# Kernel optimization log

Measured on AMD Instinct MI355X. Metric: run time of the kernel, lower is better.

Reference implementation:

```python
import jax, jax.numpy as jnp
import numpy as np

NUM_GRAPHS = 1024
N_NODES = 8388608

def setup_inputs() -> dict:
    key = jax.random.key(0)
    k1, k2, k3 = jax.random.split(key, 3)
    positions = jax.random.normal(k1, (N_NODES, 3), dtype=jnp.float32)
    q = jax.random.normal(k2, (N_NODES,), dtype=jnp.float32)
    batch = jnp.sort(jax.random.randint(k3, (N_NODES,), 0, NUM_GRAPHS, dtype=jnp.int64))
    return {"positions": positions, "q": q, "batch": batch}

def reference(positions, q, batch):
    # q: [N] -> [N,1]; remove global mean over all nodes (remove_mean=True)
    qc = q[:, None] - jnp.mean(q)
    # per-graph polarization: sum_i q_i * r_i  -> [NUM_GRAPHS, 3]
    pol = jax.ops.segment_sum(qc * positions, batch, num_segments=NUM_GRAPHS)
    return pol
```

## Files before the change

kernel.cpp:

```cpp
#include <hip/hip_runtime.h>


#define N_NODES         8388608
#define NUM_GRAPHS      1024
#define BLK             256
#define NODES_PER_BLOCK 4096
#define NBLOCKS         (N_NODES / NODES_PER_BLOCK)
#define CHUNK_NODES     1024
#define NCHUNK          (NODES_PER_BLOCK / CHUNK_NODES)
#define CHUNK_F4        (CHUNK_NODES * 3 / 4)
#define PAD4(u)         ((u) + ((u) >> 3))
#define LDS_F4          (CHUNK_F4 + (CHUNK_F4 >> 3))
#define NSLOT           4

#define IBASE_OFF       16
#define REC_OFF         2064
#define REC_STRIDE      32
#define EXTRA_OFF       (REC_OFF + NBLOCKS * REC_STRIDE)
#define WS_FLOATS       (EXTRA_OFF + NUM_GRAPHS * 6)

__global__ __launch_bounds__(BLK) void pol_main(const float4* __restrict__ p4,
                                                const float4* __restrict__ q4,
                                                const int4*   __restrict__ b4,
                                                const int*    __restrict__ batch,
                                                float* __restrict__ ws) {
    __shared__ float4 spos[LDS_F4];
    __shared__ float  sslot[NSLOT * 6];
    __shared__ float  sqsum;

    const int t = threadIdx.x;
    const int b = blockIdx.x;
    float* extra = ws + EXTRA_OFF;

    if (t == 0) sqsum = 0.f;
    if (t < NSLOT * 6) sslot[t] = 0.f;
    const int base = batch[b * NODES_PER_BLOCK];

    int idA = -1, idB = -1;
    float aqx = 0, aqy = 0, aqz = 0, arx = 0, ary = 0, arz = 0;
    float bqx = 0, bqy = 0, bqz = 0, brx = 0, bry = 0, brz = 0;
    float qsum = 0.f;

    const int blk_f4 = b * (NODES_PER_BLOCK * 3 / 4);
    const int blk_v4 = b * (NODES_PER_BLOCK / 4);

    for (int c = 0; c < NCHUNK; ++c) {
        #pragma unroll
        for (int k = 0; k < 3; ++k) {
            int u = t + BLK * k;
            spos[PAD4(u)] = p4[blk_f4 + c * CHUNK_F4 + u];
        }
        __syncthreads();

        int vi = blk_v4 + c * (CHUNK_NODES / 4) + t;
        float4 qv = q4[vi];
        int4   bv = b4[vi];
        int u0 = 3 * t;
        float4 p0 = spos[PAD4(u0)];
        float4 p1 = spos[PAD4(u0 + 1)];
        float4 p2 = spos[PAD4(u0 + 2)];

        float qs[4] = {qv.x, qv.y, qv.z, qv.w};
        int   ids[4] = {bv.x, bv.y, bv.z, bv.w};
        float px[4] = {p0.x, p0.w, p1.z, p2.y};
        float py[4] = {p0.y, p1.x, p1.w, p2.z};
        float pz[4] = {p0.z, p1.y, p2.x, p2.w};

        #pragma unroll
        for (int j = 0; j < 4; ++j) {
            float qj = qs[j];
            int   id = ids[j];
            qsum += qj;
            if (id == idA) {
                aqx = fmaf(qj, px[j], aqx); aqy = fmaf(qj, py[j], aqy); aqz = fmaf(qj, pz[j], aqz);
                arx += px[j]; ary += py[j]; arz += pz[j];
            } else if (id == idB) {
                bqx = fmaf(qj, px[j], bqx); bqy = fmaf(qj, py[j], bqy); bqz = fmaf(qj, pz[j], bqz);
                brx += px[j]; bry += py[j]; brz += pz[j];
            } else if (idA < 0) {
                idA = id;
                aqx = qj * px[j]; aqy = qj * py[j]; aqz = qj * pz[j];
                arx = px[j]; ary = py[j]; arz = pz[j];
            } else if (idB < 0) {
                idB = id;
                bqx = qj * px[j]; bqy = qj * py[j]; bqz = qj * pz[j];
                brx = px[j]; bry = py[j]; brz = pz[j];
            } else {
                atomicAdd(&extra[idA * 6 + 0], aqx); atomicAdd(&extra[idA * 6 + 1], aqy);
                atomicAdd(&extra[idA * 6 + 2], aqz); atomicAdd(&extra[idA * 6 + 3], arx);
                atomicAdd(&extra[idA * 6 + 4], ary); atomicAdd(&extra[idA * 6 + 5], arz);
                idA = id;
                aqx = qj * px[j]; aqy = qj * py[j]; aqz = qj * pz[j];
                arx = px[j]; ary = py[j]; arz = pz[j];
            }
        }
        __syncthreads();
    }

    #pragma unroll
    for (int off = 32; off > 0; off >>= 1) qsum += __shfl_down(qsum, off, 64);
    if ((t & 63) == 0) atomicAdd(&sqsum, qsum);

    {
        int s = idA - base;
        if (s < NSLOT) {
            atomicAdd(&sslot[s * 6 + 0], aqx); atomicAdd(&sslot[s * 6 + 1], aqy);
            atomicAdd(&sslot[s * 6 + 2], aqz); atomicAdd(&sslot[s * 6 + 3], arx);
            atomicAdd(&sslot[s * 6 + 4], ary); atomicAdd(&sslot[s * 6 + 5], arz);
        } else {
            atomicAdd(&extra[idA * 6 + 0], aqx); atomicAdd(&extra[idA * 6 + 1], aqy);
            atomicAdd(&extra[idA * 6 + 2], aqz); atomicAdd(&extra[idA * 6 + 3], arx);
            atomicAdd(&extra[idA * 6 + 4], ary); atomicAdd(&extra[idA * 6 + 5], arz);
        }
    }
    if (idB >= 0) {
        int s = idB - base;
        if (s < NSLOT) {
            atomicAdd(&sslot[s * 6 + 0], bqx); atomicAdd(&sslot[s * 6 + 1], bqy);
            atomicAdd(&sslot[s * 6 + 2], bqz); atomicAdd(&sslot[s * 6 + 3], brx);
            atomicAdd(&sslot[s * 6 + 4], bry); atomicAdd(&sslot[s * 6 + 5], brz);
        } else {
            atomicAdd(&extra[idB * 6 + 0], bqx); atomicAdd(&extra[idB * 6 + 1], bqy);
            atomicAdd(&extra[idB * 6 + 2], bqz); atomicAdd(&extra[idB * 6 + 3], brx);
            atomicAdd(&extra[idB * 6 + 4], bry); atomicAdd(&extra[idB * 6 + 5], brz);
        }
    }
    __syncthreads();

    float* rec = ws + REC_OFF + (size_t)b * REC_STRIDE;
    if (t == 0) {
        rec[0] = sqsum;
        ((int*)(ws + IBASE_OFF))[b] = base;
    }
    if (t < NSLOT * 6) rec[8 + t] = sslot[t];
}

__global__ __launch_bounds__(BLK) void mean_kernel(float* __restrict__ ws) {
    __shared__ float sm[4];
    float s = 0.f;
    for (int i = threadIdx.x; i < NBLOCKS; i += BLK) s += ws[REC_OFF + (size_t)i * REC_STRIDE];
    #pragma unroll
    for (int off = 32; off > 0; off >>= 1) s += __shfl_down(s, off, 64);
    int lane = threadIdx.x & 63, wave = threadIdx.x >> 6;
    if (lane == 0) sm[wave] = s;
    __syncthreads();
    if (threadIdx.x == 0) ws[0] = ((sm[0] + sm[1]) + (sm[2] + sm[3])) * (1.0f / (float)N_NODES);
}

__global__ __launch_bounds__(BLK) void finalize_kernel(const float* __restrict__ ws,
                                                       float* __restrict__ out) {
    int g = blockIdx.x * BLK + threadIdx.x;
    if (g >= NUM_GRAPHS) return;
    const float mean = ws[0];
    const int* ibase = (const int*)(ws + IBASE_OFF);
    const float* extra = ws + EXTRA_OFF;

    float qx = extra[g * 6 + 0], qy = extra[g * 6 + 1], qz = extra[g * 6 + 2];
    float rx = extra[g * 6 + 3], ry = extra[g * 6 + 4], rz = extra[g * 6 + 5];

    int lo = 0, hi = NBLOCKS - 1, B = -1;
    while (lo <= hi) {
        int mid = (lo + hi) >> 1;
        if (ibase[mid] <= g) { B = mid; lo = mid + 1; } else hi = mid - 1;
    }
    for (int b = B; b >= 0; --b) {
        int s = g - ibase[b];
        if (s >= NSLOT) break;
        const float* sl = ws + REC_OFF + (size_t)b * REC_STRIDE + 8 + s * 6;
        qx += sl[0]; qy += sl[1]; qz += sl[2];
        rx += sl[3]; ry += sl[4]; rz += sl[5];
    }
    out[g * 3 + 0] = fmaf(-mean, rx, qx);
    out[g * 3 + 1] = fmaf(-mean, ry, qy);
    out[g * 3 + 2] = fmaf(-mean, rz, qz);
}


__global__ void sum_q_kernel(const float* __restrict__ q, float* __restrict__ ws, int n4) {
    int tid = blockIdx.x * blockDim.x + threadIdx.x;
    int stride = gridDim.x * blockDim.x;
    const float4* q4 = (const float4*)q;
    float s = 0.f;
    for (int i = tid; i < n4; i += stride) {
        float4 v = q4[i];
        s += (v.x + v.y) + (v.z + v.w);
    }
    for (int off = 32; off > 0; off >>= 1) s += __shfl_down(s, off, 64);
    __shared__ float smem[4];
    int lane = threadIdx.x & 63, wave = threadIdx.x >> 6;
    if (lane == 0) smem[wave] = s;
    __syncthreads();
    if (threadIdx.x == 0) atomicAdd(ws, (smem[0] + smem[1]) + (smem[2] + smem[3]));
}

__global__ void pol_atomic_kernel(const float* __restrict__ pos,
                                  const float* __restrict__ q,
                                  const int*   __restrict__ batch,
                                  const float* __restrict__ ws,
                                  float* __restrict__ out, int n) {
    const float mean = ws[0] * (1.0f / (float)N_NODES);
    int tid = blockIdx.x * blockDim.x + threadIdx.x;
    int stride = gridDim.x * blockDim.x;
    int n4 = n >> 2;
    const float4* q4 = (const float4*)q;
    const int4*   b4 = (const int4*)batch;
    const float4* p4 = (const float4*)pos;

    for (int i = tid; i < n4; i += stride) {
        float4 qv = q4[i];
        int4   bv = b4[i];
        float4 p0 = p4[3 * i + 0];
        float4 p1 = p4[3 * i + 1];
        float4 p2 = p4[3 * i + 2];
        float qs[4] = {qv.x - mean, qv.y - mean, qv.z - mean, qv.w - mean};
        int  ids[4] = {bv.x, bv.y, bv.z, bv.w};
        float px[4] = {p0.x, p0.w, p1.z, p2.y};
        float py[4] = {p0.y, p1.x, p1.w, p2.z};
        float pz[4] = {p0.z, p1.y, p2.x, p2.w};
        int cur = ids[0];
        float sx = 0.f, sy = 0.f, sz = 0.f;
        #pragma unroll
        for (int j = 0; j < 4; ++j) {
            if (ids[j] != cur) {
                atomicAdd(&out[cur * 3 + 0], sx);
                atomicAdd(&out[cur * 3 + 1], sy);
                atomicAdd(&out[cur * 3 + 2], sz);
                sx = sy = sz = 0.f;
                cur = ids[j];
            }
            sx = fmaf(qs[j], px[j], sx);
            sy = fmaf(qs[j], py[j], sy);
            sz = fmaf(qs[j], pz[j], sz);
        }
        int first = __shfl(cur, 0, 64);
        bool uniform = __all(cur == first);
        if (uniform) {
            for (int off = 32; off > 0; off >>= 1) {
                sx += __shfl_down(sx, off, 64);
                sy += __shfl_down(sy, off, 64);
                sz += __shfl_down(sz, off, 64);
            }
            if ((threadIdx.x & 63) == 0) {
                atomicAdd(&out[cur * 3 + 0], sx);
                atomicAdd(&out[cur * 3 + 1], sy);
                atomicAdd(&out[cur * 3 + 2], sz);
            }
        } else {
            atomicAdd(&out[cur * 3 + 0], sx);
            atomicAdd(&out[cur * 3 + 1], sy);
            atomicAdd(&out[cur * 3 + 2], sz);
        }
    }
}

extern "C" void kernel_launch(void* const* d_in, const int* in_sizes, int n_in,
                              void* d_out, int out_size, void* d_ws, size_t ws_size,
                              hipStream_t stream) {
    const float* pos   = (const float*)d_in[0];
    const float* q     = (const float*)d_in[1];
    const int*   batch = (const int*)d_in[2];
    float* out = (float*)d_out;
    float* ws  = (float*)d_ws;
    int n = in_sizes[1];

    if (ws_size >= (size_t)WS_FLOATS * sizeof(float)) {
        hipMemsetAsync(ws + EXTRA_OFF, 0, (size_t)NUM_GRAPHS * 6 * sizeof(float), stream);
        pol_main<<<NBLOCKS, BLK, 0, stream>>>((const float4*)pos, (const float4*)q,
                                              (const int4*)batch, batch, ws);
        mean_kernel<<<1, BLK, 0, stream>>>(ws);
        finalize_kernel<<<NUM_GRAPHS / BLK, BLK, 0, stream>>>(ws, out);
    } else {
        hipMemsetAsync(d_out, 0, (size_t)out_size * sizeof(float), stream);
        hipMemsetAsync(d_ws, 0, sizeof(float), stream);
        sum_q_kernel<<<4096, BLK, 0, stream>>>(q, ws, n >> 2);
        pol_atomic_kernel<<<8192, BLK, 0, stream>>>(pos, q, batch, ws, out, n);
    }
}
```

Baseline: 222.8 us.

## Load positions directly, wave-reduce uniform segments, fuse mean into finalize

Removes the LDS staging of positions and its per-chunk barriers, so each thread reads its three float4 position words straight from global memory, which are contiguous per thread rather than coalesced across the wave. Before flushing, segment accumulators are reduced across the wave with shuffles when all lanes hold the same graph id, which cuts the number of shared and global atomics. The mean kernel is merged into a single 1024-thread finalize kernel, removing one launch. The risks are less efficient strided global access patterns and the extra ballot and shuffle work.

```diff
diff --git a/kernel.cpp b/kernel.cpp
--- a/kernel.cpp
+++ b/kernel.cpp
@@ -6,11 +6,7 @@
 #define BLK             256
 #define NODES_PER_BLOCK 4096
 #define NBLOCKS         (N_NODES / NODES_PER_BLOCK)
-#define CHUNK_NODES     1024
-#define NCHUNK          (NODES_PER_BLOCK / CHUNK_NODES)
-#define CHUNK_F4        (CHUNK_NODES * 3 / 4)
-#define PAD4(u)         ((u) + ((u) >> 3))
-#define LDS_F4          (CHUNK_F4 + (CHUNK_F4 >> 3))
+#define ITER            4
 #define NSLOT           4
 
 #define IBASE_OFF       16
@@ -19,14 +15,29 @@
 #define EXTRA_OFF       (REC_OFF + NBLOCKS * REC_STRIDE)
 #define WS_FLOATS       (EXTRA_OFF + NUM_GRAPHS * 6)
 
+__device__ __forceinline__ void flush_seg(int id, int base,
+                                          float qx, float qy, float qz,
+                                          float rx, float ry, float rz,
+                                          float* sslot, float* extra) {
+    int s = id - base;
+    if (s < NSLOT) {
+        atomicAdd(&sslot[s * 6 + 0], qx); atomicAdd(&sslot[s * 6 + 1], qy);
+        atomicAdd(&sslot[s * 6 + 2], qz); atomicAdd(&sslot[s * 6 + 3], rx);
+        atomicAdd(&sslot[s * 6 + 4], ry); atomicAdd(&sslot[s * 6 + 5], rz);
+    } else {
+        atomicAdd(&extra[id * 6 + 0], qx); atomicAdd(&extra[id * 6 + 1], qy);
+        atomicAdd(&extra[id * 6 + 2], qz); atomicAdd(&extra[id * 6 + 3], rx);
+        atomicAdd(&extra[id * 6 + 4], ry); atomicAdd(&extra[id * 6 + 5], rz);
+    }
+}
+
 __global__ __launch_bounds__(BLK) void pol_main(const float4* __restrict__ p4,
                                                 const float4* __restrict__ q4,
                                                 const int4*   __restrict__ b4,
                                                 const int*    __restrict__ batch,
                                                 float* __restrict__ ws) {
-    __shared__ float4 spos[LDS_F4];
-    __shared__ float  sslot[NSLOT * 6];
-    __shared__ float  sqsum;
+    __shared__ float sslot[NSLOT * 6];
+    __shared__ float sqsum;
 
     const int t = threadIdx.x;
     const int b = blockIdx.x;
@@ -35,30 +46,23 @@
     if (t == 0) sqsum = 0.f;
     if (t < NSLOT * 6) sslot[t] = 0.f;
     const int base = batch[b * NODES_PER_BLOCK];
+    __syncthreads();
 
     int idA = -1, idB = -1;
     float aqx = 0, aqy = 0, aqz = 0, arx = 0, ary = 0, arz = 0;
     float bqx = 0, bqy = 0, bqz = 0, brx = 0, bry = 0, brz = 0;
     float qsum = 0.f;
 
-    const int blk_f4 = b * (NODES_PER_BLOCK * 3 / 4);
     const int blk_v4 = b * (NODES_PER_BLOCK / 4);
 
-    for (int c = 0; c < NCHUNK; ++c) {
-        #pragma unroll
-        for (int k = 0; k < 3; ++k) {
-            int u = t + BLK * k;
-            spos[PAD4(u)] = p4[blk_f4 + c * CHUNK_F4 + u];
-        }
-        __syncthreads();
-
-        int vi = blk_v4 + c * (CHUNK_NODES / 4) + t;
+    #pragma unroll
+    for (int j = 0; j < ITER; ++j) {
+        int vi = blk_v4 + j * BLK + t;
         float4 qv = q4[vi];
         int4   bv = b4[vi];
-        int u0 = 3 * t;
-        float4 p0 = spos[PAD4(u0)];
-        float4 p1 = spos[PAD4(u0 + 1)];
-        float4 p2 = spos[PAD4(u0 + 2)];
+        float4 p0 = p4[3 * vi + 0];
+        float4 p1 = p4[3 * vi + 1];
+        float4 p2 = p4[3 * vi + 2];
 
         float qs[4] = {qv.x, qv.y, qv.z, qv.w};
         int   ids[4] = {bv.x, bv.y, bv.z, bv.w};
@@ -67,62 +71,67 @@
         float pz[4] = {p0.z, p1.y, p2.x, p2.w};
 
         #pragma unroll
-        for (int j = 0; j < 4; ++j) {
-            float qj = qs[j];
-            int   id = ids[j];
+        for (int k = 0; k < 4; ++k) {
+            float qj = qs[k];
+            int   id = ids[k];
             qsum += qj;
             if (id == idA) {
-                aqx = fmaf(qj, px[j], aqx); aqy = fmaf(qj, py[j], aqy); aqz = fmaf(qj, pz[j], aqz);
-                arx += px[j]; ary += py[j]; arz += pz[j];
+                aqx = fmaf(qj, px[k], aqx); aqy = fmaf(qj, py[k], aqy); aqz = fmaf(qj, pz[k], aqz);
+                arx += px[k]; ary += py[k]; arz += pz[k];
             } else if (id == idB) {
-                bqx = fmaf(qj, px[j], bqx); bqy = fmaf(qj, py[j], bqy); bqz = fmaf(qj, pz[j], bqz);
-                brx += px[j]; bry += py[j]; brz += pz[j];
+                bqx = fmaf(qj, px[k], bqx); bqy = fmaf(qj, py[k], bqy); bqz = fmaf(qj, pz[k], bqz);
+                brx += px[k]; bry += py[k]; brz += pz[k];
             } else if (idA < 0) {
                 idA = id;
-                aqx = qj * px[j]; aqy = qj * py[j]; aqz = qj * pz[j];
-                arx = px[j]; ary = py[j]; arz = pz[j];
+                aqx = qj * px[k]; aqy = qj * py[k]; aqz = qj * pz[k];
+                arx = px[k]; ary = py[k]; arz = pz[k];
             } else if (idB < 0) {
                 idB = id;
-                bqx = qj * px[j]; bqy = qj * py[j]; bqz = qj * pz[j];
-                brx = px[j]; bry = py[j]; brz = pz[j];
+                bqx = qj * px[k]; bqy = qj * py[k]; bqz = qj * pz[k];
+                brx = px[k]; bry = py[k]; brz = pz[k];
             } else {
                 atomicAdd(&extra[idA * 6 + 0], aqx); atomicAdd(&extra[idA * 6 + 1], aqy);
                 atomicAdd(&extra[idA * 6 + 2], aqz); atomicAdd(&extra[idA * 6 + 3], arx);
                 atomicAdd(&extra[idA * 6 + 4], ary); atomicAdd(&extra[idA * 6 + 5], arz);
                 idA = id;
-                aqx = qj * px[j]; aqy = qj * py[j]; aqz = qj * pz[j];
-                arx = px[j]; ary = py[j]; arz = pz[j];
-            }
-        }
-        __syncthreads();
+                aqx = qj * px[k]; aqy = qj * py[k]; aqz = qj * pz[k];
+                arx = px[k]; ary = py[k]; arz = pz[k];
+            }
+        }
     }
 
     #pragma unroll
     for (int off = 32; off > 0; off >>= 1) qsum += __shfl_down(qsum, off, 64);
     if ((t & 63) == 0) atomicAdd(&sqsum, qsum);
 
-    {
-        int s = idA - base;
-        if (s < NSLOT) {
-            atomicAdd(&sslot[s * 6 + 0], aqx); atomicAdd(&sslot[s * 6 + 1], aqy);
-            atomicAdd(&sslot[s * 6 + 2], aqz); atomicAdd(&sslot[s * 6 + 3], arx);
-            atomicAdd(&sslot[s * 6 + 4], ary); atomicAdd(&sslot[s * 6 + 5], arz);
-        } else {
-            atomicAdd(&extra[idA * 6 + 0], aqx); atomicAdd(&extra[idA * 6 + 1], aqy);
-            atomicAdd(&extra[idA * 6 + 2], aqz); atomicAdd(&extra[idA * 6 + 3], arx);
-            atomicAdd(&extra[idA * 6 + 4], ary); atomicAdd(&extra[idA * 6 + 5], arz);
-        }
-    }
-    if (idB >= 0) {
-        int s = idB - base;
-        if (s < NSLOT) {
-            atomicAdd(&sslot[s * 6 + 0], bqx); atomicAdd(&sslot[s * 6 + 1], bqy);
-            atomicAdd(&sslot[s * 6 + 2], bqz); atomicAdd(&sslot[s * 6 + 3], brx);
-            atomicAdd(&sslot[s * 6 + 4], bry); atomicAdd(&sslot[s * 6 + 5], brz);
-        } else {
-            atomicAdd(&extra[idB * 6 + 0], bqx); atomicAdd(&extra[idB * 6 + 1], bqy);
-            atomicAdd(&extra[idB * 6 + 2], bqz); atomicAdd(&extra[idB * 6 + 3], brx);
-            atomicAdd(&extra[idB * 6 + 4], bry); atomicAdd(&extra[idB * 6 + 5], brz);
+    bool uniA = __all(idA == __shfl(idA, 0, 64));
+    if (uniA) {
+        #pragma unroll
+        for (int off = 32; off > 0; off >>= 1) {
+            aqx += __shfl_down(aqx, off, 64); aqy += __shfl_down(aqy, off, 64);
+            aqz += __shfl_down(aqz, off, 64); arx += __shfl_down(arx, off, 64);
+            ary += __shfl_down(ary, off, 64); arz += __shfl_down(arz, off, 64);
+        }
+        if ((t & 63) == 0) flush_seg(idA, base, aqx, aqy, aqz, arx, ary, arz, sslot, extra);
+    } else {
+        flush_seg(idA, base, aqx, aqy, aqz, arx, ary, arz, sslot, extra);
+    }
+
+    unsigned long long mB = __ballot(idB >= 0);
+    if (mB) {
+        bool allB  = (mB == ~0ull);
+        int  firstB = __shfl(idB, 0, 64);
+        bool uniB  = allB && __all(idB == firstB);
+        if (uniB) {
+            #pragma unroll
+            for (int off = 32; off > 0; off >>= 1) {
+                bqx += __shfl_down(bqx, off, 64); bqy += __shfl_down(bqy, off, 64);
+                bqz += __shfl_down(bqz, off, 64); brx += __shfl_down(brx, off, 64);
+                bry += __shfl_down(bry, off, 64); brz += __shfl_down(brz, off, 64);
+            }
+            if ((t & 63) == 0) flush_seg(idB, base, bqx, bqy, bqz, brx, bry, brz, sslot, extra);
+        } else if (idB >= 0) {
+            flush_seg(idB, base, bqx, bqy, bqz, brx, bry, brz, sslot, extra);
         }
     }
     __syncthreads();
@@ -135,23 +144,28 @@
     if (t < NSLOT * 6) rec[8 + t] = sslot[t];
 }
 
-__global__ __launch_bounds__(BLK) void mean_kernel(float* __restrict__ ws) {
-    __shared__ float sm[4];
-    float s = 0.f;
-    for (int i = threadIdx.x; i < NBLOCKS; i += BLK) s += ws[REC_OFF + (size_t)i * REC_STRIDE];
+__global__ __launch_bounds__(1024) void finalize_kernel(const float* __restrict__ ws,
+                                                        float* __restrict__ out) {
+    __shared__ float sm[16];
+    __shared__ float smean;
+    const int t = threadIdx.x;
+
+    float s = ws[REC_OFF + (size_t)t * REC_STRIDE]
+            + ws[REC_OFF + (size_t)(t + 1024) * REC_STRIDE];
     #pragma unroll
     for (int off = 32; off > 0; off >>= 1) s += __shfl_down(s, off, 64);
-    int lane = threadIdx.x & 63, wave = threadIdx.x >> 6;
-    if (lane == 0) sm[wave] = s;
-    __syncthreads();
-    if (threadIdx.x == 0) ws[0] = ((sm[0] + sm[1]) + (sm[2] + sm[3])) * (1.0f / (float)N_NODES);
-}
-
-__global__ __launch_bounds__(BLK) void finalize_kernel(const float* __restrict__ ws,
-                                                       float* __restrict__ out) {
-    int g = blockIdx.x * BLK + threadIdx.x;
-    if (g >= NUM_GRAPHS) return;
-    const float mean = ws[0];
+    if ((t & 63) == 0) sm[t >> 6] = s;
+    __syncthreads();
+    if (t == 0) {
+        float tot = 0.f;
+        #pragma unroll
+        for (int i = 0; i < 16; ++i) tot += sm[i];
+        smean = tot * (1.0f / (float)N_NODES);
+    }
+    __syncthreads();
+    const float mean = smean;
+
+    const int g = t;
     const int* ibase = (const int*)(ws + IBASE_OFF);
     const float* extra = ws + EXTRA_OFF;
 
@@ -164,11 +178,11 @@
         if (ibase[mid] <= g) { B = mid; lo = mid + 1; } else hi = mid - 1;
     }
     for (int b = B; b >= 0; --b) {
-        int s = g - ibase[b];
-        if (s >= NSLOT) break;
-        const float* sl = ws + REC_OFF + (size_t)b * REC_STRIDE + 8 + s * 6;
-        qx += sl[0]; qy += sl[1]; qz += sl[2];
-        rx += sl[3]; ry += sl[4]; rz += sl[5];
+        int sl = g - ibase[b];
+        if (sl >= NSLOT) break;
+        const float* p = ws + REC_OFF + (size_t)b * REC_STRIDE + 8 + sl * 6;
+        qx += p[0]; qy += p[1]; qz += p[2];
+        rx += p[3]; ry += p[4]; rz += p[5];
     }
     out[g * 3 + 0] = fmaf(-mean, rx, qx);
     out[g * 3 + 1] = fmaf(-mean, ry, qy);
@@ -267,8 +281,7 @@
         hipMemsetAsync(ws + EXTRA_OFF, 0, (size_t)NUM_GRAPHS * 6 * sizeof(float), stream);
         pol_main<<<NBLOCKS, BLK, 0, stream>>>((const float4*)pos, (const float4*)q,
                                               (const int4*)batch, batch, ws);
-        mean_kernel<<<1, BLK, 0, stream>>>(ws);
-        finalize_kernel<<<NUM_GRAPHS / BLK, BLK, 0, stream>>>(ws, out);
+        finalize_kernel<<<1, 1024, 0, stream>>>(ws, out);
     } else {
         hipMemsetAsync(d_out, 0, (size_t)out_size * sizeof(float), stream);
         hipMemsetAsync(d_ws, 0, sizeof(float), stream);
```

New measurement: 210.3 us. 1.06x faster.
